# Performance work log

Measured on AMD Instinct MI355X. Metric: run time of the kernel, lower is better.

## Reference

```python
import jax, jax.numpy as jnp
import numpy as np

D_MODEL = 128
NUM_LAYERS = 2
D_FF = 512
VOCAB = 128
OUT_DIM = 10
B, S = 512, 256
EPS_FEAT = 1e-6
LN_EPS = 1e-5


def _pos_encoding(seq_len, d):
    pos = jnp.arange(seq_len, dtype=jnp.float32)[:, None]            # [S,1]
    div = jnp.exp(jnp.arange(0, d, 2, dtype=jnp.float32) * (-np.log(10000.0) / d))
    ang = pos * div                                                   # [S,D/2]
    pe = jnp.stack([jnp.sin(ang), jnp.cos(ang)], axis=-1).reshape(seq_len, d)
    return pe[:, None, :]                                             # [S,1,D]


def _layer_norm(x, g, b):
    mu = jnp.mean(x, axis=-1, keepdims=True)
    var = jnp.mean(jnp.square(x - mu), axis=-1, keepdims=True)
    return (x - mu) * jax.lax.rsqrt(var + LN_EPS) * g + b


def setup_inputs() -> dict:
    key = jax.random.key(0)
    ks = jax.random.split(key, 20)
    sc = 0.02
    inp = {
        'src': jax.random.randint(ks[0], (B, S), 0, VOCAB),
        'emb': jax.random.normal(ks[1], (VOCAB, D_MODEL), jnp.float32) * sc,
        'wq': jax.random.normal(ks[2], (NUM_LAYERS, D_MODEL, D_MODEL), jnp.float32) * sc,
        'bq': jnp.zeros((NUM_LAYERS, D_MODEL), jnp.float32),
        'wk': jax.random.normal(ks[3], (NUM_LAYERS, D_MODEL, D_MODEL), jnp.float32) * sc,
        'bk': jnp.zeros((NUM_LAYERS, D_MODEL), jnp.float32),
        'wv': jax.random.normal(ks[4], (NUM_LAYERS, D_MODEL, D_MODEL), jnp.float32) * sc,
        'bv': jnp.zeros((NUM_LAYERS, D_MODEL), jnp.float32),
        'w1': jax.random.normal(ks[5], (NUM_LAYERS, D_FF, D_MODEL), jnp.float32) * sc,
        'b1': jnp.zeros((NUM_LAYERS, D_FF), jnp.float32),
        'w2': jax.random.normal(ks[6], (NUM_LAYERS, D_MODEL, D_FF), jnp.float32) * sc,
        'b2': jnp.zeros((NUM_LAYERS, D_MODEL), jnp.float32),
        'g1': jnp.ones((NUM_LAYERS, D_MODEL), jnp.float32),
        'beta1': jnp.zeros((NUM_LAYERS, D_MODEL), jnp.float32),
        'g2': jnp.ones((NUM_LAYERS, D_MODEL), jnp.float32),
        'beta2': jnp.zeros((NUM_LAYERS, D_MODEL), jnp.float32),
        'fc_w': jax.random.normal(ks[7], (OUT_DIM, D_MODEL), jnp.float32) * sc,
        'fc_b': jnp.zeros((OUT_DIM,), jnp.float32),
    }
    return inp


def reference(src, emb, wq, bq, wk, bk, wv, bv, w1, b1, w2, b2,
              g1, beta1, g2, beta2, fc_w, fc_b):
    # src: [B,S] int -> permute -> [S,B]
    x = emb[src.T] * np.sqrt(float(D_MODEL))          # [S,B,D]
    x = x + _pos_encoding(x.shape[0], D_MODEL)
    for l in range(NUM_LAYERS):
        # Linear attention (faithful to original: einsum 'b' axis = seq here)
        Q = jax.nn.relu(jnp.einsum('sbd,ed->sbe', x, wq[l]) + bq[l]) + EPS_FEAT
        K = jax.nn.relu(jnp.einsum('sbd,ed->sbe', x, wk[l]) + bk[l]) + EPS_FEAT
        V = jnp.einsum('sbd,ed->sbe', x, wv[l]) + bv[l]
        KV = jnp.einsum('snd,sne->sde', K, V)         # [S,D,D] (n = batch axis)
        Z = 1.0 / (jnp.einsum('snd,sd->sn', Q, K.sum(axis=1)) + EPS_FEAT)  # [S,B]
        attn = jnp.einsum('snd,sde,sn->sne', Q, KV, Z)  # [S,B,D]
        x = _layer_norm(x + attn, g1[l], beta1[l])
        ff = jnp.einsum('sbf,df->sbd',
                        jax.nn.relu(jnp.einsum('sbd,fd->sbf', x, w1[l]) + b1[l]),
                        w2[l]) + b2[l]
        x = _layer_norm(x + ff, g2[l], beta2[l])
    x = jnp.transpose(x, (1, 0, 2))                   # [B,S,D]
    pooled = jnp.mean(x, axis=1)                      # [B,D]
    return pooled @ fc_w.T + fc_b                     # [B,OUT]
```

## Files before the change

### kernel.cpp

```cpp
#include <hip/hip_runtime.h>

typedef unsigned short u16;
typedef unsigned int u32;
typedef short bf16x8 __attribute__((ext_vector_type(8)));
typedef float f32x4 __attribute__((ext_vector_type(4)));

__device__ __forceinline__ float b2f(u16 v) { return __uint_as_float(((u32)v) << 16); }
__device__ __forceinline__ u16 f2b(float f) {
    u32 x = __float_as_uint(f);
    return (u16)((x + 0x7fffu + ((x >> 16) & 1u)) >> 16);
}
__device__ __forceinline__ float lo16(u32 w) { return __uint_as_float(w << 16); }
__device__ __forceinline__ float hi16(u32 w) { return __uint_as_float(w & 0xffff0000u); }

#define S_LEN 256
#define B_SZ  512
#define DM    128
#define DFF   512
#define MROWS (S_LEN * B_SZ)

__device__ __forceinline__ int sw16(int r, int d) {
    return r * 128 + ((((d >> 3) ^ (r & 15)) & 15) << 3) + (d & 7);
}

__global__ __launch_bounds__(256) void detect_kernel(const u32* __restrict__ embw,
                                                     int* __restrict__ flag) {
    int z = 0, big = 0;
    for (int i = threadIdx.x; i < 8192; i += 256) {
        u32 w = embw[i];
        u32 lo = w & 0xffffu;
        if (lo == 0u) z++;
        else if (((lo >> 7) & 0xffu) >= 0xC0u) big++;
    }
#pragma unroll
    for (int off = 32; off > 0; off >>= 1) {
        z   += __shfl_xor(z, off, 64);
        big += __shfl_xor(big, off, 64);
    }
    __shared__ int zz[4], bb[4];
    if ((threadIdx.x & 63) == 0) { zz[threadIdx.x >> 6] = z; bb[threadIdx.x >> 6] = big; }
    __syncthreads();
    if (threadIdx.x == 0) {
        int Z = zz[0] + zz[1] + zz[2] + zz[3];
        int Bc = bb[0] + bb[1] + bb[2] + bb[3];
        flag[0] = (Z > 4096 || Bc > 16) ? 1 : 0;
    }
}

struct Ptrs { const void* p[17]; };

__global__ __launch_bounds__(256) void convert_kernel(Ptrs ps, u16* __restrict__ canon,
                                                      const int* __restrict__ flag) {
    const int cnt[17] = {16384,32768,256,32768,256,32768,256,131072,1024,131072,
                         256,256,256,256,256,1280,10};
    const int off[17] = {0,16384,49152,49408,82176,82432,115200,115456,246528,
                         247552,378624,378880,379136,379392,379648,379904,381184};
    const int bst[18] = {0,8,24,25,41,42,58,59,123,124,188,189,190,191,192,193,194,195};
    const int isf = *flag;
    const int blk = blockIdx.x;
    int idx = 0;
#pragma unroll
    for (int i = 0; i < 17; ++i) if (blk >= bst[i + 1]) idx = i + 1;
    const int local = blk - bst[idx];
    const int n = cnt[idx];
    const void* sp = ps.p[idx];
    u16* dp = canon + off[idx];
#pragma unroll
    for (int j = 0; j < 8; ++j) {
        int e = local * 2048 + j * 256 + threadIdx.x;
        if (e < n) {
            u16 v = isf ? f2b(((const float*)sp)[e]) : ((const u16*)sp)[e];
            dp[e] = v;
        }
    }
}

__global__ __launch_bounds__(256) void embed_kernel(const int* __restrict__ src,
                                                    const u16* __restrict__ emb,
                                                    u16* __restrict__ X) {
    int idx = blockIdx.x * 256 + threadIdx.x;
    int d2 = idx & 63;
    int m = idx >> 6;
    int s = m >> 9;
    int b = m & 511;
    int tok = src[b * S_LEN + s];
    int d = d2 * 2;
    float e0 = b2f(emb[tok * DM + d])     * 11.3137084989847604f;
    float e1 = b2f(emb[tok * DM + d + 1]) * 11.3137084989847604f;
    float ang = (float)s * expf((float)d * -0.0719557841560639f);
    float v0 = e0 + sinf(ang);
    float v1 = e1 + cosf(ang);
    u32 w = (u32)f2b(v0) | ((u32)f2b(v1) << 16);
    *(u32*)(X + (size_t)m * DM + d) = w;
}

__global__ __launch_bounds__(256) void kvproj_kernel(
    const u16* __restrict__ X, const u16* __restrict__ Wk, const u16* __restrict__ bk,
    const u16* __restrict__ Wv, const u16* __restrict__ bv,
    u16* __restrict__ KVt, float* __restrict__ Ksum)
{
    __shared__ __align__(16) char sm_[49152];
    u16* Xs = (u16*)sm_;
    u16* Kt = (u16*)(sm_ + 16384);
    u16* Vt = (u16*)(sm_ + 32768);
    const int s = blockIdx.x, t = threadIdx.x;
    const int w = t >> 6, quad = (t >> 4) & 3, lr = t & 15;
    const u16* Xg = X + (size_t)s * B_SZ * DM;

    bf16x8 wkf[2][4], wvf[2][4];
    float kb[2], vb[2];
#pragma unroll
    for (int ct = 0; ct < 2; ++ct) {
        int e = w * 32 + ct * 16 + lr;
#pragma unroll
        for (int kc = 0; kc < 4; ++kc) {
            wkf[ct][kc] = *(const bf16x8*)(Wk + e * 128 + kc * 32 + quad * 8);
            wvf[ct][kc] = *(const bf16x8*)(Wv + e * 128 + kc * 32 + quad * 8);
        }
        kb[ct] = b2f(bk[e]);
        vb[ct] = b2f(bv[e]);
    }

    const f32x4 z4 = {0.f, 0.f, 0.f, 0.f};
    f32x4 kvacc[2][8];
#pragma unroll
    for (int dt = 0; dt < 2; ++dt)
#pragma unroll
        for (int ct = 0; ct < 8; ++ct) kvacc[dt][ct] = z4;
    float ks[2] = {0.f, 0.f};

    for (int b0 = 0; b0 < B_SZ; b0 += 64) {
        __syncthreads();
#pragma unroll
        for (int i = 0; i < 4; ++i) {
            int e8 = (i * 256 + t) * 8; int r = e8 >> 7, k0 = e8 & 127;
            *(uint4*)(Xs + sw16(r, k0)) = *(const uint4*)(Xg + (size_t)(b0 + r) * DM + k0);
        }
        __syncthreads();
        f32x4 pa[4][2];
#pragma unroll
        for (int mt = 0; mt < 4; ++mt) { pa[mt][0] = z4; pa[mt][1] = z4; }
#pragma unroll
        for (int kc = 0; kc < 4; ++kc) {
            bf16x8 a[4];
#pragma unroll
            for (int mt = 0; mt < 4; ++mt)
                a[mt] = *(const bf16x8*)(Xs + sw16(mt * 16 + lr, kc * 32 + quad * 8));
#pragma unroll
            for (int ct = 0; ct < 2; ++ct)
#pragma unroll
                for (int mt = 0; mt < 4; ++mt)
                    pa[mt][ct] = __builtin_amdgcn_mfma_f32_16x16x32_bf16(a[mt], wkf[ct][kc], pa[mt][ct], 0, 0, 0);
        }
#pragma unroll
        for (int ct = 0; ct < 2; ++ct) {
            int e = w * 32 + ct * 16 + lr, e7 = e & 7;
#pragma unroll
            for (int mt = 0; mt < 4; ++mt) {
                u16 h[4]; float ssum = 0.f;
#pragma unroll
                for (int j = 0; j < 4; ++j) {
                    float v = fmaxf(pa[mt][ct][j] + kb[ct], 0.f) + 1e-6f;
                    h[j] = f2b(v); ssum += b2f(h[j]);
                }
                ks[ct] += ssum;
                uint2 pk; pk.x = (u32)h[0] | ((u32)h[1] << 16); pk.y = (u32)h[2] | ((u32)h[3] << 16);
                int bs = mt * 2 + (quad >> 1);
                *(uint2*)(Kt + e * 64 + (((bs ^ e7) & 7) << 3) + (quad & 1) * 4) = pk;
            }
        }
#pragma unroll
        for (int mt = 0; mt < 4; ++mt) { pa[mt][0] = z4; pa[mt][1] = z4; }
#pragma unroll
        for (int kc = 0; kc < 4; ++kc) {
            bf16x8 a[4];
#pragma unroll
            for (int mt = 0; mt < 4; ++mt)
                a[mt] = *(const bf16x8*)(Xs + sw16(mt * 16 + lr, kc * 32 + quad * 8));
#pragma unroll
            for (int ct = 0; ct < 2; ++ct)
#pragma unroll
                for (int mt = 0; mt < 4; ++mt)
                    pa[mt][ct] = __builtin_amdgcn_mfma_f32_16x16x32_bf16(a[mt], wvf[ct][kc], pa[mt][ct], 0, 0, 0);
        }
#pragma unroll
        for (int ct = 0; ct < 2; ++ct) {
            int e = w * 32 + ct * 16 + lr, e7 = e & 7;
#pragma unroll
            for (int mt = 0; mt < 4; ++mt) {
                u16 h[4];
#pragma unroll
                for (int j = 0; j < 4; ++j) h[j] = f2b(pa[mt][ct][j] + vb[ct]);
                uint2 pk; pk.x = (u32)h[0] | ((u32)h[1] << 16); pk.y = (u32)h[2] | ((u32)h[3] << 16);
                int bs = mt * 2 + (quad >> 1);
                *(uint2*)(Vt + e * 64 + (((bs ^ e7) & 7) << 3) + (quad & 1) * 4) = pk;
            }
        }
        __syncthreads();
#pragma unroll
        for (int kc = 0; kc < 2; ++kc) {
            bf16x8 ka[2];
#pragma unroll
            for (int dt = 0; dt < 2; ++dt) {
                int d = (2 * w + dt) * 16 + lr;
                ka[dt] = *(const bf16x8*)(Kt + d * 64 + ((((kc * 4 + quad) ^ (d & 7)) & 7) << 3));
            }
#pragma unroll
            for (int ct = 0; ct < 8; ++ct) {
                int e = ct * 16 + lr;
                bf16x8 vf = *(const bf16x8*)(Vt + e * 64 + ((((kc * 4 + quad) ^ (e & 7)) & 7) << 3));
                kvacc[0][ct] = __builtin_amdgcn_mfma_f32_16x16x32_bf16(ka[0], vf, kvacc[0][ct], 0, 0, 0);
                kvacc[1][ct] = __builtin_amdgcn_mfma_f32_16x16x32_bf16(ka[1], vf, kvacc[1][ct], 0, 0, 0);
            }
        }
    }
#pragma unroll
    for (int ct = 0; ct < 2; ++ct) {
        float v = ks[ct];
        v += __shfl_xor(v, 16, 64);
        v += __shfl_xor(v, 32, 64);
        if (quad == 0) Ksum[s * 128 + w * 32 + ct * 16 + lr] = v;
    }
    u16* KVg = KVt + (size_t)s * (DM * DM);
#pragma unroll
    for (int dt = 0; dt < 2; ++dt) {
        int d0 = (2 * w + dt) * 16 + quad * 4;
#pragma unroll
        for (int ct = 0; ct < 8; ++ct) {
            int e = ct * 16 + lr;
            u16 h[4];
#pragma unroll
            for (int j = 0; j < 4; ++j) h[j] = f2b(kvacc[dt][ct][j]);
            uint2 pk; pk.x = (u32)h[0] | ((u32)h[1] << 16); pk.y = (u32)h[2] | ((u32)h[3] << 16);
            *(uint2*)(KVg + e * 128 + d0) = pk;
        }
    }
}

__global__ __launch_bounds__(256) void attn_ln_kernel(
    const u16* X, const u16* __restrict__ Wq, const u16* __restrict__ bq,
    const u16* __restrict__ KVt, const float* __restrict__ Ksum,
    u16* Xout, const u16* __restrict__ g, const u16* __restrict__ beta)
{
    __shared__ __align__(16) char sm_[65536];
    u16* R1 = (u16*)sm_;
    u16* R2 = (u16*)(sm_ + 32768);
    const int blk = blockIdx.x, s = blk >> 2, rc = blk & 3, t = threadIdx.x;
    const int w = t >> 6, quad = (t >> 4) & 3, lr = t & 15;
    const size_t m0 = (size_t)s * B_SZ + rc * 128;

#pragma unroll
    for (int i = 0; i < 8; ++i) {
        int e8 = (i * 256 + t) * 8; int r = e8 >> 7, k0 = e8 & 127;
        *(uint4*)(R1 + sw16(r, k0)) = *(const uint4*)(Wq + e8);
        *(uint4*)(R2 + sw16(r, k0)) = *(const uint4*)(X + (m0 + r) * DM + k0);
    }
    __syncthreads();
    const f32x4 z4 = {0.f, 0.f, 0.f, 0.f};
    f32x4 qacc[2][8];
#pragma unroll
    for (int mt = 0; mt < 2; ++mt)
#pragma unroll
        for (int ct = 0; ct < 8; ++ct) qacc[mt][ct] = z4;
#pragma unroll
    for (int kc = 0; kc < 4; ++kc) {
        bf16x8 a[2];
#pragma unroll
        for (int mt = 0; mt < 2; ++mt)
            a[mt] = *(const bf16x8*)(R2 + sw16(w * 32 + mt * 16 + lr, kc * 32 + quad * 8));
#pragma unroll
        for (int ct = 0; ct < 8; ++ct) {
            bf16x8 wf = *(const bf16x8*)(R1 + sw16(ct * 16 + lr, kc * 32 + quad * 8));
            qacc[0][ct] = __builtin_amdgcn_mfma_f32_16x16x32_bf16(a[0], wf, qacc[0][ct], 0, 0, 0);
            qacc[1][ct] = __builtin_amdgcn_mfma_f32_16x16x32_bf16(a[1], wf, qacc[1][ct], 0, 0, 0);
        }
    }
    __syncthreads();
    float ksm[8], bqv[8];
#pragma unroll
    for (int ct = 0; ct < 8; ++ct) {
        ksm[ct] = Ksum[s * 128 + ct * 16 + lr];
        bqv[ct] = b2f(bq[ct * 16 + lr]);
    }
    float zden[2][4];
#pragma unroll
    for (int mt = 0; mt < 2; ++mt)
#pragma unroll
        for (int j = 0; j < 4; ++j) zden[mt][j] = 0.f;
#pragma unroll
    for (int mt = 0; mt < 2; ++mt)
#pragma unroll
        for (int ct = 0; ct < 8; ++ct) {
            int d = ct * 16 + lr;
#pragma unroll
            for (int j = 0; j < 4; ++j) {
                float qv = fmaxf(qacc[mt][ct][j] + bqv[ct], 0.f) + 1e-6f;
                u16 qb16 = f2b(qv);
                zden[mt][j] += b2f(qb16) * ksm[ct];
                int b = w * 32 + mt * 16 + quad * 4 + j;
                R1[sw16(b, d)] = qb16;
            }
        }
#pragma unroll
    for (int mt = 0; mt < 2; ++mt)
#pragma unroll
        for (int j = 0; j < 4; ++j) {
            float v = zden[mt][j];
            v += __shfl_xor(v, 1, 64); v += __shfl_xor(v, 2, 64);
            v += __shfl_xor(v, 4, 64); v += __shfl_xor(v, 8, 64);
            zden[mt][j] = 1.f / (v + 1e-6f);
        }
    const u16* KVg = KVt + (size_t)s * (DM * DM);
#pragma unroll
    for (int i = 0; i < 8; ++i) {
        int e8 = (i * 256 + t) * 8; int r = e8 >> 7, k0 = e8 & 127;
        *(uint4*)(R2 + sw16(r, k0)) = *(const uint4*)(KVg + e8);
    }
    __syncthreads();
    f32x4 oacc[2][8];
#pragma unroll
    for (int mt = 0; mt < 2; ++mt)
#pragma unroll
        for (int ct = 0; ct < 8; ++ct) oacc[mt][ct] = z4;
#pragma unroll
    for (int kc = 0; kc < 4; ++kc) {
        bf16x8 qa[2];
#pragma unroll
        for (int mt = 0; mt < 2; ++mt)
            qa[mt] = *(const bf16x8*)(R1 + sw16(w * 32 + mt * 16 + lr, kc * 32 + quad * 8));
#pragma unroll
        for (int ct = 0; ct < 8; ++ct) {
            bf16x8 kf = *(const bf16x8*)(R2 + sw16(ct * 16 + lr, kc * 32 + quad * 8));
            oacc[0][ct] = __builtin_amdgcn_mfma_f32_16x16x32_bf16(qa[0], kf, oacc[0][ct], 0, 0, 0);
            oacc[1][ct] = __builtin_amdgcn_mfma_f32_16x16x32_bf16(qa[1], kf, oacc[1][ct], 0, 0, 0);
        }
    }
    float gv[8], bev[8];
#pragma unroll
    for (int ct = 0; ct < 8; ++ct) {
        gv[ct]  = b2f(g[ct * 16 + lr]);
        bev[ct] = b2f(beta[ct * 16 + lr]);
    }
#pragma unroll
    for (int mt = 0; mt < 2; ++mt)
#pragma unroll
        for (int j = 0; j < 4; ++j) {
            int b = w * 32 + mt * 16 + quad * 4 + j;
            const u16* xr = X + (m0 + b) * DM;
            float vals[8], sum = 0.f, sq = 0.f;
#pragma unroll
            for (int ct = 0; ct < 8; ++ct) {
                float v = fmaf(oacc[mt][ct][j], zden[mt][j], b2f(xr[ct * 16 + lr]));
                vals[ct] = v; sum += v; sq += v * v;
            }
            sum += __shfl_xor(sum, 1, 64); sq += __shfl_xor(sq, 1, 64);
            sum += __shfl_xor(sum, 2, 64); sq += __shfl_xor(sq, 2, 64);
            sum += __shfl_xor(sum, 4, 64); sq += __shfl_xor(sq, 4, 64);
            sum += __shfl_xor(sum, 8, 64); sq += __shfl_xor(sq, 8, 64);
            float mean = sum * 0.0078125f;
            float var  = sq * 0.0078125f - mean * mean;
            float rstd = rsqrtf(fmaxf(var, 0.f) + 1e-5f);
            u16* xo = Xout + (m0 + b) * DM;
#pragma unroll
            for (int ct = 0; ct < 8; ++ct)
                xo[ct * 16 + lr] = f2b((vals[ct] - mean) * rstd * gv[ct] + bev[ct]);
        }
}

__global__ __launch_bounds__(256, 4) void mlp_kernel(
    const u16* X, const u16* __restrict__ W1, const u16* __restrict__ b1,
    const u16* __restrict__ W2, const u16* __restrict__ b2,
    u16* Xout, const u16* __restrict__ g, const u16* __restrict__ beta)
{
    __shared__ __align__(16) char sm_[40960];
    u16* W1c = (u16*)sm_;
    u16* W2c = (u16*)(sm_ + 16384);
    u16* Hc  = (u16*)(sm_ + 32768);
    const int t = threadIdx.x;
    const int m0 = blockIdx.x * 64;
    const int w  = t >> 6;
    const int quad = (t >> 4) & 3;
    const int lr = t & 15;

    bf16x8 af[4];
    {
        const u16* xr = X + (size_t)(m0 + w * 16 + lr) * DM + quad * 8;
#pragma unroll
        for (int kc = 0; kc < 4; ++kc)
            af[kc] = *(const bf16x8*)(xr + kc * 32);
    }

    const f32x4 zero4 = {0.f, 0.f, 0.f, 0.f};
    f32x4 zacc[8];
#pragma unroll
    for (int ct = 0; ct < 8; ++ct) zacc[ct] = zero4;

    for (int fc = 0; fc < DFF; fc += 64) {
        __syncthreads();
#pragma unroll
        for (int i = 0; i < 4; ++i) {
            int e = (i * 256 + t) * 8; int c = e >> 7, k0 = e & 127;
            *(uint4*)(W1c + sw16(c, k0)) = *(const uint4*)(W1 + (size_t)(fc + c) * DM + k0);
        }
#pragma unroll
        for (int i = 0; i < 4; ++i) {
            int e = (i * 256 + t) * 8; int d = e >> 6, f0 = e & 63, sl = f0 >> 3;
            *(uint4*)(W2c + d * 64 + (((sl ^ (d & 7)) & 7) << 3)) =
                *(const uint4*)(W2 + (size_t)d * DFF + fc + f0);
        }
        __syncthreads();
        f32x4 hacc[4];
#pragma unroll
        for (int ct = 0; ct < 4; ++ct) hacc[ct] = zero4;
#pragma unroll
        for (int kc = 0; kc < 4; ++kc)
#pragma unroll
            for (int ct = 0; ct < 4; ++ct) {
                bf16x8 bf_ = *(const bf16x8*)(W1c + sw16(ct * 16 + lr, kc * 32 + quad * 8));
                hacc[ct] = __builtin_amdgcn_mfma_f32_16x16x32_bf16(af[kc], bf_, hacc[ct], 0, 0, 0);
            }
#pragma unroll
        for (int ct = 0; ct < 4; ++ct) {
            int f = ct * 16 + lr;
            float hbv = b2f(b1[fc + f]);
#pragma unroll
            for (int j = 0; j < 4; ++j) {
                int m = w * 16 + quad * 4 + j;
                float v = fmaxf(hacc[ct][j] + hbv, 0.f);
                Hc[m * 64 + ((((f >> 3) ^ (m & 7)) & 7) << 3) + (f & 7)] = f2b(v);
            }
        }
#pragma unroll
        for (int kc = 0; kc < 2; ++kc) {
            int m = w * 16 + lr;
            bf16x8 ha = *(const bf16x8*)(Hc + m * 64 + ((((kc * 4 + quad) ^ (m & 7)) & 7) << 3));
#pragma unroll
            for (int ct = 0; ct < 8; ++ct) {
                int d = ct * 16 + lr;
                bf16x8 wb = *(const bf16x8*)(W2c + d * 64 + ((((kc * 4 + quad) ^ (d & 7)) & 7) << 3));
                zacc[ct] = __builtin_amdgcn_mfma_f32_16x16x32_bf16(ha, wb, zacc[ct], 0, 0, 0);
            }
        }
    }
    float gv[8], bev[8], bbv[8];
#pragma unroll
    for (int ct = 0; ct < 8; ++ct) {
        gv[ct]  = b2f(g[ct * 16 + lr]);
        bev[ct] = b2f(beta[ct * 16 + lr]);
        bbv[ct] = b2f(b2[ct * 16 + lr]);
    }
#pragma unroll
    for (int j = 0; j < 4; ++j) {
        int m = w * 16 + quad * 4 + j;
        const u16* xr = X + (size_t)(m0 + m) * DM;
        float vals[8], sum = 0.f, sq = 0.f;
#pragma unroll
        for (int ct = 0; ct < 8; ++ct) {
            float v = zacc[ct][j] + bbv[ct] + b2f(xr[ct * 16 + lr]);
            vals[ct] = v; sum += v; sq += v * v;
        }
        sum += __shfl_xor(sum, 1, 64); sq += __shfl_xor(sq, 1, 64);
        sum += __shfl_xor(sum, 2, 64); sq += __shfl_xor(sq, 2, 64);
        sum += __shfl_xor(sum, 4, 64); sq += __shfl_xor(sq, 4, 64);
        sum += __shfl_xor(sum, 8, 64); sq += __shfl_xor(sq, 8, 64);
        float mean = sum * 0.0078125f;
        float var  = sq * 0.0078125f - mean * mean;
        float rstd = rsqrtf(fmaxf(var, 0.f) + 1e-5f);
        u16* xo = Xout + (size_t)(m0 + m) * DM;
#pragma unroll
        for (int ct = 0; ct < 8; ++ct)
            xo[ct * 16 + lr] = f2b((vals[ct] - mean) * rstd * gv[ct] + bev[ct]);
    }
}

__global__ __launch_bounds__(128) void pool_fc_kernel(
    const u16* __restrict__ X, const u16* __restrict__ fcw,
    const u16* __restrict__ fcb, void* __restrict__ Out,
    const int* __restrict__ flag)
{
    __shared__ float pool[128];
    const int b = blockIdx.x, t = threadIdx.x;
    float acc = 0.f;
    for (int s = 0; s < S_LEN; ++s)
        acc += b2f(X[((size_t)s * B_SZ + b) * DM + t]);
    pool[t] = acc * (1.0f / 256.0f);
    __syncthreads();
    if (t < 10) {
        float o = b2f(fcb[t]);
        for (int d = 0; d < 128; ++d) o += pool[d] * b2f(fcw[t * 128 + d]);
        if (*flag) ((float*)Out)[b * 10 + t] = o;
        else       ((u16*)Out)[b * 10 + t] = f2b(o);
    }
}

extern "C" void kernel_launch(void* const* d_in, const int* in_sizes, int n_in,
                              void* d_out, int out_size, void* d_ws, size_t ws_size,
                              hipStream_t stream)
{
    const int* src = (const int*)d_in[0];

    char* ws = (char*)d_ws;
    u16*   X    = (u16*)ws;
    u16*   KVt  = (u16*)(ws + 33554432);
    float* Ksum = (float*)(ws + 41943040);
    int*   flag = (int*)(ws + 42074112);
    u16*   cn   = (u16*)(ws + 42074368);

    u16* emb = cn + 0;
    u16* wq  = cn + 16384;
    u16* bq  = cn + 49152;
    u16* wk  = cn + 49408;
    u16* bk  = cn + 82176;
    u16* wv  = cn + 82432;
    u16* bvp = cn + 115200;
    u16* w1  = cn + 115456;
    u16* b1  = cn + 246528;
    u16* w2  = cn + 247552;
    u16* b2  = cn + 378624;
    u16* g1  = cn + 378880;
    u16* be1 = cn + 379136;
    u16* g2  = cn + 379392;
    u16* be2 = cn + 379648;
    u16* fcw = cn + 379904;
    u16* fcb = cn + 381184;

    detect_kernel<<<1, 256, 0, stream>>>((const u32*)d_in[1], flag);

    Ptrs ps;
    for (int i = 0; i < 17; ++i) ps.p[i] = d_in[i + 1];
    convert_kernel<<<195, 256, 0, stream>>>(ps, cn, flag);

    embed_kernel<<<MROWS * 64 / 256, 256, 0, stream>>>(src, emb, X);

    for (int l = 0; l < 2; ++l) {
        kvproj_kernel<<<S_LEN, 256, 0, stream>>>(
            X, wk + l * DM * DM, bk + l * DM, wv + l * DM * DM, bvp + l * DM, KVt, Ksum);
        attn_ln_kernel<<<S_LEN * 4, 256, 0, stream>>>(
            X, wq + l * DM * DM, bq + l * DM, KVt, Ksum, X, g1 + l * DM, be1 + l * DM);
        mlp_kernel<<<MROWS / 64, 256, 0, stream>>>(
            X, w1 + l * DFF * DM, b1 + l * DFF, w2 + l * DM * DFF, b2 + l * DM,
            X, g2 + l * DM, be2 + l * DM);
    }

    pool_fc_kernel<<<B_SZ, 128, 0, stream>>>(X, fcw, fcb, d_out, flag);
}
```

Before: 434.0 us.

## Double-buffer MLP weight chunks and process 128 rows per block

The MLP kernel now handles 128 rows per block in two groups, so each weight tile loaded into shared memory is reused across twice as many rows. The DFF loop switches to 32-wide chunks with register-prefetched, double-buffered shared-memory weight tiles, which removes one barrier per iteration and overlaps global loads with MFMA work. A new swizzle is added for the 32-wide tiles. The costs are higher register pressure (launch bounds lowered to 3 blocks per CU) and half as many blocks in the grid.

```diff
diff --git a/kernel.cpp b/kernel.cpp
--- a/kernel.cpp
+++ b/kernel.cpp
@@ -21,6 +21,9 @@
 
 __device__ __forceinline__ int sw16(int r, int d) {
     return r * 128 + ((((d >> 3) ^ (r & 15)) & 15) << 3) + (d & 7);
+}
+__device__ __forceinline__ int sw32(int r, int f) {
+    return r * 32 + ((((f >> 3) ^ (r & 3) ^ ((r >> 2) & 3)) & 3) << 3) + (f & 7);
 }
 
 __global__ __launch_bounds__(256) void detect_kernel(const u32* __restrict__ embw,
@@ -367,81 +370,109 @@
         }
 }
 
-__global__ __launch_bounds__(256, 4) void mlp_kernel(
+__global__ __launch_bounds__(256, 3) void mlp_kernel(
     const u16* X, const u16* __restrict__ W1, const u16* __restrict__ b1,
     const u16* __restrict__ W2, const u16* __restrict__ b2,
     u16* Xout, const u16* __restrict__ g, const u16* __restrict__ beta)
 {
     __shared__ __align__(16) char sm_[40960];
-    u16* W1c = (u16*)sm_;
-    u16* W2c = (u16*)(sm_ + 16384);
-    u16* Hc  = (u16*)(sm_ + 32768);
+    u16* Hc = (u16*)(sm_ + 32768);
     const int t = threadIdx.x;
-    const int m0 = blockIdx.x * 64;
+    const int m0 = blockIdx.x * 128;
     const int w  = t >> 6;
     const int quad = (t >> 4) & 3;
     const int lr = t & 15;
 
-    bf16x8 af[4];
+    bf16x8 af[2][4];
+#pragma unroll
+    for (int gr = 0; gr < 2; ++gr) {
+        const u16* xr = X + (size_t)(m0 + gr * 64 + w * 16 + lr) * DM + quad * 8;
+#pragma unroll
+        for (int kc = 0; kc < 4; ++kc)
+            af[gr][kc] = *(const bf16x8*)(xr + kc * 32);
+    }
+
+    const f32x4 zero4 = {0.f, 0.f, 0.f, 0.f};
+    f32x4 zacc[2][8];
+#pragma unroll
+    for (int gr = 0; gr < 2; ++gr)
+#pragma unroll
+        for (int ct = 0; ct < 8; ++ct) zacc[gr][ct] = zero4;
+
+    uint4 rw1[2], rw2[2];
+#pragma unroll
+    for (int i = 0; i < 2; ++i) {
+        int e = (i * 256 + t) * 8;
+        rw1[i] = *(const uint4*)(W1 + (size_t)(e >> 7) * DM + (e & 127));
+        rw2[i] = *(const uint4*)(W2 + (size_t)(e >> 5) * DFF + (e & 31));
+    }
     {
-        const u16* xr = X + (size_t)(m0 + w * 16 + lr) * DM + quad * 8;
+        u16* w1b = (u16*)sm_;
+        u16* w2b = w1b + 4096;
+#pragma unroll
+        for (int i = 0; i < 2; ++i) {
+            int e = (i * 256 + t) * 8;
+            *(uint4*)(w1b + sw16(e >> 7, e & 127)) = rw1[i];
+            *(uint4*)(w2b + sw32(e >> 5, e & 31)) = rw2[i];
+        }
+    }
+    __syncthreads();
+
+    for (int fc = 0; fc < 16; ++fc) {
+        const int cur = fc & 1;
+        u16* w1c = (u16*)(sm_ + cur * 16384);
+        u16* w2c = w1c + 4096;
+        if (fc < 15) {
+#pragma unroll
+            for (int i = 0; i < 2; ++i) {
+                int e = (i * 256 + t) * 8;
+                rw1[i] = *(const uint4*)(W1 + (size_t)((fc + 1) * 32 + (e >> 7)) * DM + (e & 127));
+                rw2[i] = *(const uint4*)(W2 + (size_t)(e >> 5) * DFF + (fc + 1) * 32 + (e & 31));
+            }
+        }
+        f32x4 ha_[2][2];
+        ha_[0][0] = zero4; ha_[0][1] = zero4; ha_[1][0] = zero4; ha_[1][1] = zero4;
 #pragma unroll
         for (int kc = 0; kc < 4; ++kc)
-            af[kc] = *(const bf16x8*)(xr + kc * 32);
-    }
-
-    const f32x4 zero4 = {0.f, 0.f, 0.f, 0.f};
-    f32x4 zacc[8];
-#pragma unroll
-    for (int ct = 0; ct < 8; ++ct) zacc[ct] = zero4;
-
-    for (int fc = 0; fc < DFF; fc += 64) {
+#pragma unroll
+            for (int ct = 0; ct < 2; ++ct) {
+                bf16x8 bf_ = *(const bf16x8*)(w1c + sw16(ct * 16 + lr, kc * 32 + quad * 8));
+                ha_[0][ct] = __builtin_amdgcn_mfma_f32_16x16x32_bf16(af[0][kc], bf_, ha_[0][ct], 0, 0, 0);
+                ha_[1][ct] = __builtin_amdgcn_mfma_f32_16x16x32_bf16(af[1][kc], bf_, ha_[1][ct], 0, 0, 0);
+            }
+#pragma unroll
+        for (int gr = 0; gr < 2; ++gr)
+#pragma unroll
+            for (int ct = 0; ct < 2; ++ct) {
+                int f = ct * 16 + lr;
+                float hbv = b2f(b1[fc * 32 + f]);
+#pragma unroll
+                for (int j = 0; j < 4; ++j) {
+                    int m = gr * 64 + w * 16 + quad * 4 + j;
+                    Hc[sw32(m, f)] = f2b(fmaxf(ha_[gr][ct][j] + hbv, 0.f));
+                }
+            }
+        bf16x8 h0 = *(const bf16x8*)(Hc + sw32(w * 16 + lr, quad * 8));
+        bf16x8 h1 = *(const bf16x8*)(Hc + sw32(64 + w * 16 + lr, quad * 8));
+#pragma unroll
+        for (int ct = 0; ct < 8; ++ct) {
+            bf16x8 wb = *(const bf16x8*)(w2c + sw32(ct * 16 + lr, quad * 8));
+            zacc[0][ct] = __builtin_amdgcn_mfma_f32_16x16x32_bf16(h0, wb, zacc[0][ct], 0, 0, 0);
+            zacc[1][ct] = __builtin_amdgcn_mfma_f32_16x16x32_bf16(h1, wb, zacc[1][ct], 0, 0, 0);
+        }
+        if (fc < 15) {
+            u16* w1n = (u16*)(sm_ + (cur ^ 1) * 16384);
+            u16* w2n = w1n + 4096;
+#pragma unroll
+            for (int i = 0; i < 2; ++i) {
+                int e = (i * 256 + t) * 8;
+                *(uint4*)(w1n + sw16(e >> 7, e & 127)) = rw1[i];
+                *(uint4*)(w2n + sw32(e >> 5, e & 31)) = rw2[i];
+            }
+        }
         __syncthreads();
-#pragma unroll
-        for (int i = 0; i < 4; ++i) {
-            int e = (i * 256 + t) * 8; int c = e >> 7, k0 = e & 127;
-            *(uint4*)(W1c + sw16(c, k0)) = *(const uint4*)(W1 + (size_t)(fc + c) * DM + k0);
-        }
-#pragma unroll
-        for (int i = 0; i < 4; ++i) {
-            int e = (i * 256 + t) * 8; int d = e >> 6, f0 = e & 63, sl = f0 >> 3;
-            *(uint4*)(W2c + d * 64 + (((sl ^ (d & 7)) & 7) << 3)) =
-                *(const uint4*)(W2 + (size_t)d * DFF + fc + f0);
-        }
-        __syncthreads();
-        f32x4 hacc[4];
-#pragma unroll
-        for (int ct = 0; ct < 4; ++ct) hacc[ct] = zero4;
-#pragma unroll
-        for (int kc = 0; kc < 4; ++kc)
-#pragma unroll
-            for (int ct = 0; ct < 4; ++ct) {
-                bf16x8 bf_ = *(const bf16x8*)(W1c + sw16(ct * 16 + lr, kc * 32 + quad * 8));
-                hacc[ct] = __builtin_amdgcn_mfma_f32_16x16x32_bf16(af[kc], bf_, hacc[ct], 0, 0, 0);
-            }
-#pragma unroll
-        for (int ct = 0; ct < 4; ++ct) {
-            int f = ct * 16 + lr;
-            float hbv = b2f(b1[fc + f]);
-#pragma unroll
-            for (int j = 0; j < 4; ++j) {
-                int m = w * 16 + quad * 4 + j;
-                float v = fmaxf(hacc[ct][j] + hbv, 0.f);
-                Hc[m * 64 + ((((f >> 3) ^ (m & 7)) & 7) << 3) + (f & 7)] = f2b(v);
-            }
-        }
-#pragma unroll
-        for (int kc = 0; kc < 2; ++kc) {
-            int m = w * 16 + lr;
-            bf16x8 ha = *(const bf16x8*)(Hc + m * 64 + ((((kc * 4 + quad) ^ (m & 7)) & 7) << 3));
-#pragma unroll
-            for (int ct = 0; ct < 8; ++ct) {
-                int d = ct * 16 + lr;
-                bf16x8 wb = *(const bf16x8*)(W2c + d * 64 + ((((kc * 4 + quad) ^ (d & 7)) & 7) << 3));
-                zacc[ct] = __builtin_amdgcn_mfma_f32_16x16x32_bf16(ha, wb, zacc[ct], 0, 0, 0);
-            }
-        }
-    }
+    }
+
     float gv[8], bev[8], bbv[8];
 #pragma unroll
     for (int ct = 0; ct < 8; ++ct) {
@@ -450,27 +481,29 @@
         bbv[ct] = b2f(b2[ct * 16 + lr]);
     }
 #pragma unroll
-    for (int j = 0; j < 4; ++j) {
-        int m = w * 16 + quad * 4 + j;
-        const u16* xr = X + (size_t)(m0 + m) * DM;
-        float vals[8], sum = 0.f, sq = 0.f;
-#pragma unroll
-        for (int ct = 0; ct < 8; ++ct) {
-            float v = zacc[ct][j] + bbv[ct] + b2f(xr[ct * 16 + lr]);
-            vals[ct] = v; sum += v; sq += v * v;
-        }
-        sum += __shfl_xor(sum, 1, 64); sq += __shfl_xor(sq, 1, 64);
-        sum += __shfl_xor(sum, 2, 64); sq += __shfl_xor(sq, 2, 64);
-        sum += __shfl_xor(sum, 4, 64); sq += __shfl_xor(sq, 4, 64);
-        sum += __shfl_xor(sum, 8, 64); sq += __shfl_xor(sq, 8, 64);
-        float mean = sum * 0.0078125f;
-        float var  = sq * 0.0078125f - mean * mean;
-        float rstd = rsqrtf(fmaxf(var, 0.f) + 1e-5f);
-        u16* xo = Xout + (size_t)(m0 + m) * DM;
-#pragma unroll
-        for (int ct = 0; ct < 8; ++ct)
-            xo[ct * 16 + lr] = f2b((vals[ct] - mean) * rstd * gv[ct] + bev[ct]);
-    }
+    for (int gr = 0; gr < 2; ++gr)
+#pragma unroll
+        for (int j = 0; j < 4; ++j) {
+            int m = gr * 64 + w * 16 + quad * 4 + j;
+            const u16* xr = X + (size_t)(m0 + m) * DM;
+            float vals[8], sum = 0.f, sq = 0.f;
+#pragma unroll
+            for (int ct = 0; ct < 8; ++ct) {
+                float v = zacc[gr][ct][j] + bbv[ct] + b2f(xr[ct * 16 + lr]);
+                vals[ct] = v; sum += v; sq += v * v;
+            }
+            sum += __shfl_xor(sum, 1, 64); sq += __shfl_xor(sq, 1, 64);
+            sum += __shfl_xor(sum, 2, 64); sq += __shfl_xor(sq, 2, 64);
+            sum += __shfl_xor(sum, 4, 64); sq += __shfl_xor(sq, 4, 64);
+            sum += __shfl_xor(sum, 8, 64); sq += __shfl_xor(sq, 8, 64);
+            float mean = sum * 0.0078125f;
+            float var  = sq * 0.0078125f - mean * mean;
+            float rstd = rsqrtf(fmaxf(var, 0.f) + 1e-5f);
+            u16* xo = Xout + (size_t)(m0 + m) * DM;
+#pragma unroll
+            for (int ct = 0; ct < 8; ++ct)
+                xo[ct * 16 + lr] = f2b((vals[ct] - mean) * rstd * gv[ct] + bev[ct]);
+        }
 }
 
 __global__ __launch_bounds__(128) void pool_fc_kernel(
@@ -537,7 +570,7 @@
             X, wk + l * DM * DM, bk + l * DM, wv + l * DM * DM, bvp + l * DM, KVt, Ksum);
         attn_ln_kernel<<<S_LEN * 4, 256, 0, stream>>>(
             X, wq + l * DM * DM, bq + l * DM, KVt, Ksum, X, g1 + l * DM, be1 + l * DM);
-        mlp_kernel<<<MROWS / 64, 256, 0, stream>>>(
+        mlp_kernel<<<MROWS / 128, 256, 0, stream>>>(
             X, w1 + l * DFF * DM, b1 + l * DFF, w2 + l * DM * DFF, b2 + l * DM,
             X, g2 + l * DM, be2 + l * DM);
     }
```

After: 438.6 us. No clear change (+1.1%).

## Prefetch next FFN weight chunk into registers while computing current chunk

Applied to the files above, without the earlier changes.

The fused FFN kernel now loads the next 64-column chunk of W1/W2 and b1 from global memory into registers before running the MFMAs on the current chunk, then writes them to LDS after a barrier. This overlaps global load latency with tensor-core compute instead of stalling at the top of each chunk iteration. It costs extra registers per thread, which may lower occupancy.

```diff
diff --git a/kernel.cpp b/kernel.cpp
--- a/kernel.cpp
+++ b/kernel.cpp
@@ -395,20 +395,40 @@
 #pragma unroll
     for (int ct = 0; ct < 8; ++ct) zacc[ct] = zero4;
 
+    uint4 rw1[4], rw2[4];
+    u16 rb[4];
+
+#pragma unroll
+    for (int i = 0; i < 4; ++i) {
+        int e = (i * 256 + t) * 8;
+        rw1[i] = *(const uint4*)(W1 + (size_t)(e >> 7) * DM + (e & 127));
+        rw2[i] = *(const uint4*)(W2 + (size_t)(e >> 6) * DFF + (e & 63));
+    }
+#pragma unroll
+    for (int ct = 0; ct < 4; ++ct) rb[ct] = b1[ct * 16 + lr];
+#pragma unroll
+    for (int i = 0; i < 4; ++i) {
+        int e = (i * 256 + t) * 8;
+        *(uint4*)(W1c + sw16(e >> 7, e & 127)) = rw1[i];
+        int d = e >> 6, f0 = e & 63, sl = f0 >> 3;
+        *(uint4*)(W2c + d * 64 + (((sl ^ (d & 7)) & 7) << 3)) = rw2[i];
+    }
+    __syncthreads();
+
     for (int fc = 0; fc < DFF; fc += 64) {
-        __syncthreads();
-#pragma unroll
-        for (int i = 0; i < 4; ++i) {
-            int e = (i * 256 + t) * 8; int c = e >> 7, k0 = e & 127;
-            *(uint4*)(W1c + sw16(c, k0)) = *(const uint4*)(W1 + (size_t)(fc + c) * DM + k0);
-        }
-#pragma unroll
-        for (int i = 0; i < 4; ++i) {
-            int e = (i * 256 + t) * 8; int d = e >> 6, f0 = e & 63, sl = f0 >> 3;
-            *(uint4*)(W2c + d * 64 + (((sl ^ (d & 7)) & 7) << 3)) =
-                *(const uint4*)(W2 + (size_t)d * DFF + fc + f0);
-        }
-        __syncthreads();
+        u16 rbc[4];
+#pragma unroll
+        for (int ct = 0; ct < 4; ++ct) rbc[ct] = rb[ct];
+        if (fc < DFF - 64) {
+#pragma unroll
+            for (int i = 0; i < 4; ++i) {
+                int e = (i * 256 + t) * 8;
+                rw1[i] = *(const uint4*)(W1 + (size_t)(fc + 64 + (e >> 7)) * DM + (e & 127));
+                rw2[i] = *(const uint4*)(W2 + (size_t)(e >> 6) * DFF + fc + 64 + (e & 63));
+            }
+#pragma unroll
+            for (int ct = 0; ct < 4; ++ct) rb[ct] = b1[fc + 64 + ct * 16 + lr];
+        }
         f32x4 hacc[4];
 #pragma unroll
         for (int ct = 0; ct < 4; ++ct) hacc[ct] = zero4;
@@ -422,7 +442,7 @@
 #pragma unroll
         for (int ct = 0; ct < 4; ++ct) {
             int f = ct * 16 + lr;
-            float hbv = b2f(b1[fc + f]);
+            float hbv = b2f(rbc[ct]);
 #pragma unroll
             for (int j = 0; j < 4; ++j) {
                 int m = w * 16 + quad * 4 + j;
@@ -441,7 +461,19 @@
                 zacc[ct] = __builtin_amdgcn_mfma_f32_16x16x32_bf16(ha, wb, zacc[ct], 0, 0, 0);
             }
         }
-    }
+        __syncthreads();
+        if (fc < DFF - 64) {
+#pragma unroll
+            for (int i = 0; i < 4; ++i) {
+                int e = (i * 256 + t) * 8;
+                *(uint4*)(W1c + sw16(e >> 7, e & 127)) = rw1[i];
+                int d = e >> 6, f0 = e & 63, sl = f0 >> 3;
+                *(uint4*)(W2c + d * 64 + (((sl ^ (d & 7)) & 7) << 3)) = rw2[i];
+            }
+            __syncthreads();
+        }
+    }
+
     float gv[8], bev[8], bbv[8];
 #pragma unroll
     for (int ct = 0; ct < 8; ++ct) {
```

New measurement: 610.8 us. +40.8%, slower.

## Keep weight fragments in registers and stage activations in LDS for MLP kernel

Applied to the files above, without the earlier changes.

The MLP kernel now loads each chunk's W1/W2 fragments straight from global memory into registers per wave, where they were previously cooperatively copied into LDS. The 64-row activation tile goes into LDS with async global_load_lds, and each wave computes a slice of the hidden and output features across all rows. The epilogue stages output through LDS so the layernorm runs with coalesced row-wise stores. This aims to cut LDS weight traffic and scattered 2-byte stores, but occupancy drops to 3 blocks and global weight loads are no longer shared across waves.

```diff
diff --git a/kernel.cpp b/kernel.cpp
--- a/kernel.cpp
+++ b/kernel.cpp
@@ -12,6 +12,13 @@
 }
 __device__ __forceinline__ float lo16(u32 w) { return __uint_as_float(w << 16); }
 __device__ __forceinline__ float hi16(u32 w) { return __uint_as_float(w & 0xffff0000u); }
+
+__device__ __forceinline__ void gld_lds16(const u16* g, u16* l) {
+    __builtin_amdgcn_global_load_lds(
+        (const __attribute__((address_space(1))) unsigned int*)g,
+        (__attribute__((address_space(3))) unsigned int*)l,
+        16, 0, 0);
+}
 
 #define S_LEN 256
 #define B_SZ  512
@@ -367,109 +374,115 @@
         }
 }
 
-__global__ __launch_bounds__(256, 4) void mlp_kernel(
+__global__ __launch_bounds__(256, 3) void mlp_kernel(
     const u16* X, const u16* __restrict__ W1, const u16* __restrict__ b1,
     const u16* __restrict__ W2, const u16* __restrict__ b2,
     u16* Xout, const u16* __restrict__ g, const u16* __restrict__ beta)
 {
-    __shared__ __align__(16) char sm_[40960];
-    u16* W1c = (u16*)sm_;
-    u16* W2c = (u16*)(sm_ + 16384);
-    u16* Hc  = (u16*)(sm_ + 32768);
+    __shared__ __align__(16) char sm_[32768];
+    u16* Xs = (u16*)sm_;
+    u16* Hc = (u16*)(sm_ + 16384);
+    float* zs = (float*)sm_;
     const int t = threadIdx.x;
     const int m0 = blockIdx.x * 64;
     const int w  = t >> 6;
     const int quad = (t >> 4) & 3;
     const int lr = t & 15;
-
-    bf16x8 af[4];
-    {
-        const u16* xr = X + (size_t)(m0 + w * 16 + lr) * DM + quad * 8;
+    const int l  = t & 63;
+
+#pragma unroll
+    for (int i = 0; i < 4; ++i) {
+        int r = i * 16 + (t >> 4);
+        int sslot = (t & 15) ^ (r & 15);
+        gld_lds16(X + (size_t)(m0 + r) * DM + (sslot << 3),
+                  Xs + i * 2048 + w * 512);
+    }
+
+    const f32x4 zero4 = {0.f, 0.f, 0.f, 0.f};
+    f32x4 zacc[4][2];
+#pragma unroll
+    for (int mt = 0; mt < 4; ++mt) { zacc[mt][0] = zero4; zacc[mt][1] = zero4; }
+
+    __syncthreads();
+
+    for (int fc = 0; fc < DFF; fc += 64) {
+        bf16x8 w1f[4];
 #pragma unroll
         for (int kc = 0; kc < 4; ++kc)
-            af[kc] = *(const bf16x8*)(xr + kc * 32);
-    }
-
-    const f32x4 zero4 = {0.f, 0.f, 0.f, 0.f};
-    f32x4 zacc[8];
-#pragma unroll
-    for (int ct = 0; ct < 8; ++ct) zacc[ct] = zero4;
-
-    for (int fc = 0; fc < DFF; fc += 64) {
+            w1f[kc] = *(const bf16x8*)(W1 + (size_t)(fc + w * 16 + lr) * DM + kc * 32 + quad * 8);
+        bf16x8 w2f[2][2];
+#pragma unroll
+        for (int ct = 0; ct < 2; ++ct)
+#pragma unroll
+            for (int kc = 0; kc < 2; ++kc)
+                w2f[ct][kc] = *(const bf16x8*)(W2 + (size_t)(w * 32 + ct * 16 + lr) * DFF + fc + kc * 32 + quad * 8);
+        float hb[4];
+#pragma unroll
+        for (int j = 0; j < 4; ++j)
+            hb[j] = b2f(b1[fc + w * 16 + quad * 4 + j]);
+
+        f32x4 hacc[4];
+#pragma unroll
+        for (int mt = 0; mt < 4; ++mt) hacc[mt] = zero4;
+#pragma unroll
+        for (int kc = 0; kc < 4; ++kc)
+#pragma unroll
+            for (int mt = 0; mt < 4; ++mt) {
+                bf16x8 xb = *(const bf16x8*)(Xs + sw16(mt * 16 + lr, kc * 32 + quad * 8));
+                hacc[mt] = __builtin_amdgcn_mfma_f32_16x16x32_bf16(w1f[kc], xb, hacc[mt], 0, 0, 0);
+            }
+#pragma unroll
+        for (int mt = 0; mt < 4; ++mt) {
+            int m = mt * 16 + lr;
+            int f0 = w * 16 + quad * 4;
+            u16 h[4];
+#pragma unroll
+            for (int j = 0; j < 4; ++j)
+                h[j] = f2b(fmaxf(hacc[mt][j] + hb[j], 0.f));
+            uint2 pk; pk.x = (u32)h[0] | ((u32)h[1] << 16); pk.y = (u32)h[2] | ((u32)h[3] << 16);
+            *(uint2*)(Hc + m * 64 + ((((f0 >> 3) ^ (m & 7)) & 7) << 3) + (f0 & 7)) = pk;
+        }
         __syncthreads();
 #pragma unroll
-        for (int i = 0; i < 4; ++i) {
-            int e = (i * 256 + t) * 8; int c = e >> 7, k0 = e & 127;
-            *(uint4*)(W1c + sw16(c, k0)) = *(const uint4*)(W1 + (size_t)(fc + c) * DM + k0);
-        }
-#pragma unroll
-        for (int i = 0; i < 4; ++i) {
-            int e = (i * 256 + t) * 8; int d = e >> 6, f0 = e & 63, sl = f0 >> 3;
-            *(uint4*)(W2c + d * 64 + (((sl ^ (d & 7)) & 7) << 3)) =
-                *(const uint4*)(W2 + (size_t)d * DFF + fc + f0);
-        }
+        for (int kc = 0; kc < 2; ++kc)
+#pragma unroll
+            for (int mt = 0; mt < 4; ++mt) {
+                int m = mt * 16 + lr;
+                bf16x8 ha = *(const bf16x8*)(Hc + m * 64 + ((((kc * 4 + quad) ^ (m & 7)) & 7) << 3));
+                zacc[mt][0] = __builtin_amdgcn_mfma_f32_16x16x32_bf16(ha, w2f[0][kc], zacc[mt][0], 0, 0, 0);
+                zacc[mt][1] = __builtin_amdgcn_mfma_f32_16x16x32_bf16(ha, w2f[1][kc], zacc[mt][1], 0, 0, 0);
+            }
         __syncthreads();
-        f32x4 hacc[4];
-#pragma unroll
-        for (int ct = 0; ct < 4; ++ct) hacc[ct] = zero4;
-#pragma unroll
-        for (int kc = 0; kc < 4; ++kc)
-#pragma unroll
-            for (int ct = 0; ct < 4; ++ct) {
-                bf16x8 bf_ = *(const bf16x8*)(W1c + sw16(ct * 16 + lr, kc * 32 + quad * 8));
-                hacc[ct] = __builtin_amdgcn_mfma_f32_16x16x32_bf16(af[kc], bf_, hacc[ct], 0, 0, 0);
-            }
-#pragma unroll
-        for (int ct = 0; ct < 4; ++ct) {
-            int f = ct * 16 + lr;
-            float hbv = b2f(b1[fc + f]);
-#pragma unroll
-            for (int j = 0; j < 4; ++j) {
-                int m = w * 16 + quad * 4 + j;
-                float v = fmaxf(hacc[ct][j] + hbv, 0.f);
-                Hc[m * 64 + ((((f >> 3) ^ (m & 7)) & 7) << 3) + (f & 7)] = f2b(v);
-            }
-        }
-#pragma unroll
-        for (int kc = 0; kc < 2; ++kc) {
-            int m = w * 16 + lr;
-            bf16x8 ha = *(const bf16x8*)(Hc + m * 64 + ((((kc * 4 + quad) ^ (m & 7)) & 7) << 3));
-#pragma unroll
-            for (int ct = 0; ct < 8; ++ct) {
-                int d = ct * 16 + lr;
-                bf16x8 wb = *(const bf16x8*)(W2c + d * 64 + ((((kc * 4 + quad) ^ (d & 7)) & 7) << 3));
-                zacc[ct] = __builtin_amdgcn_mfma_f32_16x16x32_bf16(ha, wb, zacc[ct], 0, 0, 0);
-            }
-        }
-    }
-    float gv[8], bev[8], bbv[8];
-#pragma unroll
-    for (int ct = 0; ct < 8; ++ct) {
-        gv[ct]  = b2f(g[ct * 16 + lr]);
-        bev[ct] = b2f(beta[ct * 16 + lr]);
-        bbv[ct] = b2f(b2[ct * 16 + lr]);
-    }
-#pragma unroll
-    for (int j = 0; j < 4; ++j) {
-        int m = w * 16 + quad * 4 + j;
-        const u16* xr = X + (size_t)(m0 + m) * DM;
-        float vals[8], sum = 0.f, sq = 0.f;
-#pragma unroll
-        for (int ct = 0; ct < 8; ++ct) {
-            float v = zacc[ct][j] + bbv[ct] + b2f(xr[ct * 16 + lr]);
-            vals[ct] = v; sum += v; sq += v * v;
-        }
-        sum += __shfl_xor(sum, 1, 64); sq += __shfl_xor(sq, 1, 64);
-        sum += __shfl_xor(sum, 2, 64); sq += __shfl_xor(sq, 2, 64);
-        sum += __shfl_xor(sum, 4, 64); sq += __shfl_xor(sq, 4, 64);
-        sum += __shfl_xor(sum, 8, 64); sq += __shfl_xor(sq, 8, 64);
+    }
+
+    float bbv[2] = { b2f(b2[w * 32 + lr]), b2f(b2[w * 32 + 16 + lr]) };
+#pragma unroll
+    for (int mt = 0; mt < 4; ++mt)
+#pragma unroll
+        for (int ct = 0; ct < 2; ++ct)
+#pragma unroll
+            for (int j = 0; j < 4; ++j)
+                zs[(mt * 16 + quad * 4 + j) * 128 + w * 32 + ct * 16 + lr] =
+                    zacc[mt][ct][j] + bbv[ct];
+    __syncthreads();
+
+    float g0 = b2f(g[l]), g1v = b2f(g[64 + l]);
+    float be0 = b2f(beta[l]), be1 = b2f(beta[64 + l]);
+    for (int q = 0; q < 16; ++q) {
+        int r = w * 16 + q;
+        float v0 = zs[r * 128 + l]      + b2f(X[(size_t)(m0 + r) * DM + l]);
+        float v1 = zs[r * 128 + 64 + l] + b2f(X[(size_t)(m0 + r) * DM + 64 + l]);
+        float sum = v0 + v1, sq = v0 * v0 + v1 * v1;
+#pragma unroll
+        for (int off = 32; off > 0; off >>= 1) {
+            sum += __shfl_xor(sum, off, 64);
+            sq  += __shfl_xor(sq,  off, 64);
+        }
         float mean = sum * 0.0078125f;
         float var  = sq * 0.0078125f - mean * mean;
         float rstd = rsqrtf(fmaxf(var, 0.f) + 1e-5f);
-        u16* xo = Xout + (size_t)(m0 + m) * DM;
-#pragma unroll
-        for (int ct = 0; ct < 8; ++ct)
-            xo[ct * 16 + lr] = f2b((vals[ct] - mean) * rstd * gv[ct] + bev[ct]);
+        Xout[(size_t)(m0 + r) * DM + l]      = f2b((v0 - mean) * rstd * g0  + be0);
+        Xout[(size_t)(m0 + r) * DM + 64 + l] = f2b((v1 - mean) * rstd * g1v + be1);
     }
 }
 
```

After: 457.4 us. 1.05x slower.
